# Kernel tuning notes

Hardware: AMD Instinct MI355X
Metric: run time of the kernel (lower is better)

Reference implementation:

```python
import jax, jax.numpy as jnp
import numpy as np

N_HEADS = 8
D_K = 64
NEG = 1e9


def setup_inputs() -> dict:
    key = jax.random.key(0)
    k1, k2, k3 = jax.random.split(key, 3)
    B, L, C = 4, 2048, 512
    x = jax.random.normal(k1, (B, L, C), dtype=jnp.float32)
    W_in = jax.random.normal(k2, (C, N_HEADS * D_K * 3), dtype=jnp.float32) * (C ** -0.5)
    b_in = jnp.zeros((N_HEADS * D_K * 3,), dtype=jnp.float32)
    W_out = jax.random.normal(k3, (N_HEADS * D_K, C), dtype=jnp.float32) * ((N_HEADS * D_K) ** -0.5)
    b_out = jnp.zeros((C,), dtype=jnp.float32)
    return {"x": x, "W_in": W_in, "b_in": b_in, "W_out": W_out, "b_out": b_out}


def reference(x, W_in, b_in, W_out, b_out):
    B, L, C = x.shape
    H, Dk = N_HEADS, D_K
    scale = Dk ** -0.5
    qkv = x @ W_in + b_in                       # [B, L, 3*H*Dk]
    qkv = qkv.reshape(B, L, H, 3 * Dk)
    q, k, v = jnp.split(qkv, 3, axis=-1)         # each [B, L, H, Dk]
    attn = jnp.einsum('bihd,bjhd->bijh', q, k) * scale  # [B, L, L, H]
    mask = jnp.tril(jnp.ones((L, L), dtype=x.dtype))[None, :, :, None]
    attn = attn * mask - NEG * (1.0 - mask)
    attn = jax.nn.softmax(attn, axis=2)          # softmax over j
    res = jnp.einsum('bijh,bjhd->bihd', attn, v)  # [B, L, H, Dk]
    res = res.reshape(B, L, H * Dk)
    res = res @ W_out + b_out
    return res + x
```

## Files before the change

### kernel.cpp

```cpp
#include <hip/hip_runtime.h>
#include <hip/hip_bf16.h>
#include <math.h>
#include <cstddef>
#include <cstring>


constexpr int B_SZ  = 4;
constexpr int L_SEQ = 2048;
constexpr int C_DIM = 512;
constexpr int H_N   = 8;
constexpr int DK    = 64;
constexpr int N_QKV = 1536;
constexpr int M_ROWS = B_SZ * L_SEQ;
constexpr float SCALE = 0.125f;
constexpr float DEFER_THR = 8.f;

typedef __attribute__((ext_vector_type(4))) float f32x4;
typedef __attribute__((ext_vector_type(8))) short bf16x8;
typedef __attribute__((ext_vector_type(4))) unsigned int u32x4;

static __device__ inline ushort f2bf(float f) {
  unsigned u = __builtin_bit_cast(unsigned, f);
  u += 0x7fffu + ((u >> 16) & 1u);
  return (ushort)(u >> 16);
}

static __device__ inline unsigned pack_bf2(float a, float b) {
  const __hip_bfloat162 v = __float22bfloat162_rn(make_float2(a, b));
  unsigned u;
  __builtin_memcpy(&u, &v, 4);
  return u;
}

typedef __attribute__((address_space(1))) const unsigned int* gas1_t;
typedef __attribute__((address_space(3))) unsigned int* las3_t;
static __device__ inline void gload_lds16(const void* g, void* l) {
  __builtin_amdgcn_global_load_lds((gas1_t)g, (las3_t)l, 16, 0, 0);
}


__global__ __launch_bounds__(256) void prep_w(
    const float* __restrict__ W_in, const float* __restrict__ W_out,
    ushort* __restrict__ WinT, ushort* __restrict__ WoutT) {
  __shared__ ushort T[64][65];
  const int id = blockIdx.x;
  const float* src;
  ushort* dst;
  int R, C, c0, r0;
  if (id < 192) {
    src = W_in; dst = WinT; R = C_DIM; C = N_QKV;
    c0 = (id % 24) * 64; r0 = (id / 24) * 64;
  } else {
    const int t = id - 192;
    src = W_out; dst = WoutT; R = C_DIM; C = C_DIM;
    c0 = (t % 8) * 64; r0 = (t / 8) * 64;
  }
#pragma unroll
  for (int p = 0; p < 16; ++p) {
    const int idx = threadIdx.x + p * 256;
    const int r = idx >> 6, c = idx & 63;
    T[r][c] = f2bf(src[(size_t)(r0 + r) * C + c0 + c]);
  }
  __syncthreads();
#pragma unroll
  for (int p = 0; p < 16; ++p) {
    const int idx = threadIdx.x + p * 256;
    const int r = idx >> 6, c = idx & 63;
    dst[(size_t)(c0 + r) * R + r0 + c] = T[c][r];
  }
}

__global__ __launch_bounds__(256) void gemm_qkv(
    const float* __restrict__ Af, const ushort* __restrict__ Bt,
    const float* __restrict__ bias, ushort* __restrict__ Qo,
    ushort* __restrict__ Ko, ushort* __restrict__ Vto, int N, int K, int nbx) {
  __shared__ float Alf[128 * 32];
  __shared__ ushort Bl[128 * 32];
  const int id = blockIdx.x;
  const int xcd = id & 7, i = id >> 3;
  const int bn = (i % nbx) * 128;
  const int bm = (xcd * 8 + i / nbx) * 128;
  const int tid = threadIdx.x;
  const int w = tid >> 6, l = tid & 63;
  const int cc = l & 15, gg = l >> 4;
  const int wr = w >> 1, wc = w & 1;
  f32x4 acc[4][4] = {};

  for (int k0 = 0; k0 < K; k0 += 32) {
#pragma unroll
    for (int q = 0; q < 4; ++q) {
      const int cidx = q * 256 + tid;
      const int row = cidx >> 3, pc = cidx & 7;
      gload_lds16(Af + (size_t)(bm + row) * K + k0 + ((pc ^ (row & 7)) << 2),
                  &Alf[(q * 256 + w * 64) * 4]);
    }
#pragma unroll
    for (int q = 0; q < 2; ++q) {
      const int cbase = q * 256 + w * 64;
      const int c = cbase + l;
      gload_lds16(Bt + (size_t)(bn + (c >> 2)) * K + k0 + (c & 3) * 8,
                  &Bl[cbase * 8]);
    }
    __syncthreads();
    bf16x8 aF[4], bF[4];
#pragma unroll
    for (int i2 = 0; i2 < 4; ++i2) {
      const int rowA = wr * 64 + i2 * 16 + cc;
      const float4 fa = *reinterpret_cast<const float4*>(
          &Alf[rowA * 32 + (((2 * gg) ^ (cc & 7)) << 2)]);
      const float4 fb = *reinterpret_cast<const float4*>(
          &Alf[rowA * 32 + (((2 * gg + 1) ^ (cc & 7)) << 2)]);
      u32x4 up;
      up[0] = pack_bf2(fa.x, fa.y);
      up[1] = pack_bf2(fa.z, fa.w);
      up[2] = pack_bf2(fb.x, fb.y);
      up[3] = pack_bf2(fb.z, fb.w);
      aF[i2] = __builtin_bit_cast(bf16x8, up);
    }
#pragma unroll
    for (int j = 0; j < 4; ++j)
      bF[j] = *reinterpret_cast<const bf16x8*>(
          &Bl[(wc * 64 + j * 16 + cc) * 32 + gg * 8]);
#pragma unroll
    for (int i2 = 0; i2 < 4; ++i2)
#pragma unroll
      for (int j = 0; j < 4; ++j)
        acc[i2][j] = __builtin_amdgcn_mfma_f32_16x16x32_bf16(aF[i2], bF[j],
                                                             acc[i2][j], 0, 0, 0);
    __syncthreads();
  }

#pragma unroll
  for (int j = 0; j < 4; ++j) {
    const int colbase = bn + wc * 64 + j * 16;
    const int h = colbase / 192, rem = colbase % 192;
    const int type = rem / 64, d = (rem % 64) + cc;
    const float bv = bias[colbase + cc];
#pragma unroll
    for (int i2 = 0; i2 < 4; ++i2) {
      const int rowbase = bm + wr * 64 + i2 * 16 + 4 * gg;
      const int b = rowbase >> 11, ll = rowbase & 2047;
      const size_t bh32 = (size_t)(b * H_N + h) * 32;
      if (type == 0) {
#pragma unroll
        for (int r = 0; r < 4; ++r)
          Qo[((size_t)(b * H_N + h) * L_SEQ + ll + r) * DK + d] =
              f2bf(acc[i2][j][r] + bv);
      } else if (type == 1) {
#pragma unroll
        for (int r = 0; r < 4; ++r) {
          const int jg = ll + r;
          Ko[(bh32 + (jg >> 6)) * 4096 + (jg & 63) * 64 +
             (((d >> 3) ^ (jg & 7)) << 3) + (d & 7)] =
              f2bf(acc[i2][j][r] + bv);
        }
      } else {
        ushort4 pk;
        pk.x = f2bf(acc[i2][j][0] + bv);
        pk.y = f2bf(acc[i2][j][1] + bv);
        pk.z = f2bf(acc[i2][j][2] + bv);
        pk.w = f2bf(acc[i2][j][3] + bv);
        const size_t idx = (bh32 + (ll >> 6)) * 4096 + (size_t)d * 64 +
                           ((((ll & 63) >> 3) ^ (d & 7)) << 3) + (ll & 7);
        *reinterpret_cast<ushort4*>(&Vto[idx]) = pk;
      }
    }
  }
}

__global__ __launch_bounds__(256) void gemm_out(
    const ushort* __restrict__ A, const ushort* __restrict__ Bt,
    const float* __restrict__ bias, float* __restrict__ outF,
    const float* __restrict__ resid, int N, int K, int nbx) {
  __shared__ ushort Al[64 * 32];
  __shared__ ushort Bl[64 * 32];
  const int id = blockIdx.x;
  const int xcd = id & 7, i = id >> 3;
  const int bn = (i % nbx) * 64;
  const int bm = (xcd * 16 + i / nbx) * 64;
  const int tid = threadIdx.x;
  const int w = tid >> 6, l = tid & 63;
  const int cc = l & 15, gg = l >> 4;
  const int wr = w >> 1, wc = w & 1;
  f32x4 acc[2][2] = {};

  for (int k0 = 0; k0 < K; k0 += 32) {
    {
      const int c = w * 64 + l;
      gload_lds16(A + (size_t)(bm + (c >> 2)) * K + k0 + (c & 3) * 8,
                  &Al[(w * 64) * 8]);
    }
    {
      const int c = w * 64 + l;
      gload_lds16(Bt + (size_t)(bn + (c >> 2)) * K + k0 + (c & 3) * 8,
                  &Bl[(w * 64) * 8]);
    }
    __syncthreads();
    bf16x8 aF[2], bF[2];
#pragma unroll
    for (int i2 = 0; i2 < 2; ++i2)
      aF[i2] = *reinterpret_cast<const bf16x8*>(
          &Al[(wr * 32 + i2 * 16 + cc) * 32 + gg * 8]);
#pragma unroll
    for (int j = 0; j < 2; ++j)
      bF[j] = *reinterpret_cast<const bf16x8*>(
          &Bl[(wc * 32 + j * 16 + cc) * 32 + gg * 8]);
#pragma unroll
    for (int i2 = 0; i2 < 2; ++i2)
#pragma unroll
      for (int j = 0; j < 2; ++j)
        acc[i2][j] = __builtin_amdgcn_mfma_f32_16x16x32_bf16(aF[i2], bF[j],
                                                             acc[i2][j], 0, 0, 0);
    __syncthreads();
  }

#pragma unroll
  for (int j = 0; j < 2; ++j) {
    const int col = bn + wc * 32 + j * 16 + cc;
    const float bv = bias[col];
#pragma unroll
    for (int i2 = 0; i2 < 2; ++i2) {
      const int rowbase = bm + wr * 32 + i2 * 16 + 4 * gg;
#pragma unroll
      for (int r = 0; r < 4; ++r) {
        const size_t off = (size_t)(rowbase + r) * N + col;
        outF[off] = acc[i2][j][r] + bv + resid[off];
      }
    }
  }
}

#define STAGE(buf, tile)                                                     \
  {                                                                          \
    const ushort* kg_ = KoB + (size_t)(tile) * 4096 + w * 1024 + lane * 8;   \
    const ushort* vg_ = VtB + (size_t)(tile) * 4096 + w * 1024 + lane * 8;   \
    gload_lds16(kg_, &Ks[buf][w * 1024]);                                    \
    gload_lds16(kg_ + 512, &Ks[buf][w * 1024 + 512]);                        \
    gload_lds16(vg_, &Vs[buf][w * 1024]);                                    \
    gload_lds16(vg_ + 512, &Vs[buf][w * 1024 + 512]);                        \
  }

__global__ __launch_bounds__(256, 4) void attn_mfma(
    const ushort* __restrict__ Q, const ushort* __restrict__ Ko,
    const ushort* __restrict__ Vt, ushort* __restrict__ attn_out) {
  __shared__ ushort Ks[2][4096];
  __shared__ ushort Vs[2][4096];
  __shared__ ushort Pw_s[4][1024];
  const int id = blockIdx.x;
  const int bh = (id & 7) + 8 * ((id >> 3) & 3);
  const int qt = 31 - (id >> 5);
  const int tid = threadIdx.x;
  const int w = tid >> 6, lane = tid & 63;
  const int c = lane & 15, g = lane >> 4;
  const int b = bh >> 3, h = bh & 7;
  const ushort* KoB = Ko + (size_t)bh * 32 * 4096;
  const ushort* VtB = Vt + (size_t)bh * 32 * 4096;
  const int q0 = qt * 64 + w * 16;
  ushort* Pw = Pw_s[w];
  const int pc0 = (g ^ (c & 7)) * 8;
  const int pc1 = ((g + 4) ^ (c & 7)) * 8;

  bf16x8 qA[2];
  {
    const ushort* qp = Q + ((size_t)bh * L_SEQ + q0 + c) * DK + g * 8;
    qA[0] = *reinterpret_cast<const bf16x8*>(qp);
    qA[1] = *reinterpret_cast<const bf16x8*>(qp + 32);
  }

  f32x4 O[4] = {};
  float mrow[4] = {-INFINITY, -INFINITY, -INFINITY, -INFINITY};
  float lsum[4] = {};
  const f32x4 zero4 = {0.f, 0.f, 0.f, 0.f};

  STAGE(0, 0);
  __syncthreads();

  for (int jt = 0; jt <= qt; ++jt) {
    const int cur = jt & 1;
    if (jt < qt) STAGE(cur ^ 1, jt + 1);
    const ushort* Kc = Ks[cur];
    const ushort* Vc = Vs[cur];
    const int j0 = jt * 64;
    f32x4 S[4];
#pragma unroll
    for (int n = 0; n < 4; ++n) {
      const bf16x8 k0 = *reinterpret_cast<const bf16x8*>(&Kc[(n * 16 + c) * 64 + pc0]);
      const bf16x8 k1 = *reinterpret_cast<const bf16x8*>(&Kc[(n * 16 + c) * 64 + pc1]);
      S[n] = __builtin_amdgcn_mfma_f32_16x16x32_bf16(qA[0], k0, zero4, 0, 0, 0);
      S[n] = __builtin_amdgcn_mfma_f32_16x16x32_bf16(qA[1], k1, S[n], 0, 0, 0);
    }
    const bool diag = (jt == qt);
#pragma unroll
    for (int n = 0; n < 4; ++n)
#pragma unroll
      for (int r = 0; r < 4; ++r) {
        float v = S[n][r] * SCALE;
        if (diag && (j0 + n * 16 + c) > (q0 + 4 * g + r)) v = -INFINITY;
        S[n][r] = v;
      }
    float pm[4];
    int exceed = 0;
#pragma unroll
    for (int r = 0; r < 4; ++r) {
      pm[r] = fmaxf(fmaxf(S[0][r], S[1][r]), fmaxf(S[2][r], S[3][r]));
      exceed |= (pm[r] > mrow[r] + DEFER_THR);
    }
    if (__any(exceed)) {
#pragma unroll
      for (int r = 0; r < 4; ++r) {
        float fm = pm[r];
        fm = fmaxf(fm, __shfl_xor(fm, 1, 16));
        fm = fmaxf(fm, __shfl_xor(fm, 2, 16));
        fm = fmaxf(fm, __shfl_xor(fm, 4, 16));
        fm = fmaxf(fm, __shfl_xor(fm, 8, 16));
        const float mnew = fmaxf(mrow[r], fm);
        const float corr = __expf(mrow[r] - mnew);
        lsum[r] *= corr;
#pragma unroll
        for (int t = 0; t < 4; ++t) O[t][r] *= corr;
        mrow[r] = mnew;
      }
    }
#pragma unroll
    for (int n = 0; n < 4; ++n)
#pragma unroll
      for (int r = 0; r < 4; ++r) {
        const float p = __expf(S[n][r] - mrow[r]);
        S[n][r] = p;
        lsum[r] += p;
      }
#pragma unroll
    for (int n = 0; n < 4; ++n)
#pragma unroll
      for (int r = 0; r < 4; ++r) {
        const int row = 4 * g + r;
        Pw[row * 64 + ((2 * n + (c >> 3)) ^ (row & 7)) * 8 + (c & 7)] =
            f2bf(S[n][r]);
      }
    const bf16x8 pA0 = *reinterpret_cast<const bf16x8*>(&Pw[c * 64 + pc0]);
    const bf16x8 pA1 = *reinterpret_cast<const bf16x8*>(&Pw[c * 64 + pc1]);
#pragma unroll
    for (int t = 0; t < 4; ++t) {
      const bf16x8 v0 = *reinterpret_cast<const bf16x8*>(&Vc[(t * 16 + c) * 64 + pc0]);
      const bf16x8 v1 = *reinterpret_cast<const bf16x8*>(&Vc[(t * 16 + c) * 64 + pc1]);
      O[t] = __builtin_amdgcn_mfma_f32_16x16x32_bf16(pA0, v0, O[t], 0, 0, 0);
      O[t] = __builtin_amdgcn_mfma_f32_16x16x32_bf16(pA1, v1, O[t], 0, 0, 0);
    }
    __syncthreads();
  }
  float inv[4];
#pragma unroll
  for (int r = 0; r < 4; ++r) {
    float s = lsum[r];
    s += __shfl_xor(s, 1, 16);
    s += __shfl_xor(s, 2, 16);
    s += __shfl_xor(s, 4, 16);
    s += __shfl_xor(s, 8, 16);
    inv[r] = 1.f / s;
  }
#pragma unroll
  for (int t = 0; t < 4; ++t)
#pragma unroll
    for (int r = 0; r < 4; ++r)
      attn_out[((size_t)b * L_SEQ + q0 + 4 * g + r) * C_DIM + h * DK + t * 16 + c] =
          f2bf(O[t][r] * inv[r]);
}

extern "C" void kernel_launch(void* const* d_in, const int* in_sizes, int n_in,
                              void* d_out, int out_size, void* d_ws,
                              size_t ws_size, hipStream_t stream) {
  const float* x     = (const float*)d_in[0];
  const float* W_in  = (const float*)d_in[1];
  const float* b_in  = (const float*)d_in[2];
  const float* W_out = (const float*)d_in[3];
  const float* b_out = (const float*)d_in[4];
  float* out = (float*)d_out;

  ushort* WinT  = (ushort*)d_ws;
  ushort* WoutT = WinT + (size_t)N_QKV * C_DIM;
  ushort* Qo    = WoutT + (size_t)C_DIM * C_DIM;
  ushort* Ko    = Qo + (size_t)M_ROWS * C_DIM;
  ushort* Vto   = Ko + (size_t)M_ROWS * C_DIM;
  ushort* attnb = Vto + (size_t)M_ROWS * C_DIM;

  prep_w<<<dim3(256, 1, 1), 256, 0, stream>>>(W_in, W_out, WinT, WoutT);
  gemm_qkv<<<dim3(768, 1, 1), 256, 0, stream>>>(
      x, WinT, b_in, Qo, Ko, Vto, N_QKV, C_DIM, 12);
  attn_mfma<<<dim3(1024, 1, 1), 256, 0, stream>>>(Qo, Ko, Vto, attnb);
  gemm_out<<<dim3(1024, 1, 1), 256, 0, stream>>>(
      attnb, WoutT, b_out, out, x, C_DIM, C_DIM, 8);
}
```

Baseline: 86.83 us.

## Double-buffer LDS tiles in QKV and output GEMMs to overlap loads

Both projection GEMMs now keep two shared-memory buffers and issue the async global-to-LDS loads for the next K tile before computing on the current one. This is meant to hide global load latency behind the MFMA work. It doubles LDS use per block, which may lower occupancy. Correctness depends on the remaining end-of-iteration barrier and on the compiler inserting the right vmcnt waits for the direct-to-LDS loads.

```diff
diff --git a/kernel.cpp b/kernel.cpp
--- a/kernel.cpp
+++ b/kernel.cpp
@@ -70,12 +70,31 @@
   }
 }
 
+#define STAGE_G1(buf, k0)                                                    \
+  {                                                                          \
+    _Pragma("unroll")                                                        \
+    for (int q_ = 0; q_ < 4; ++q_) {                                         \
+      const int cidx_ = q_ * 256 + tid;                                      \
+      const int row_ = cidx_ >> 3, pc_ = cidx_ & 7;                          \
+      gload_lds16(                                                           \
+          Af + (size_t)(bm + row_) * K + (k0) + ((pc_ ^ (row_ & 7)) << 2),   \
+          &Alf[buf][(q_ * 256 + w * 64) * 4]);                               \
+    }                                                                        \
+    _Pragma("unroll")                                                        \
+    for (int q_ = 0; q_ < 2; ++q_) {                                         \
+      const int cbase_ = q_ * 256 + w * 64;                                  \
+      const int c_ = cbase_ + l;                                             \
+      gload_lds16(Bt + (size_t)(bn + (c_ >> 2)) * K + (k0) + (c_ & 3) * 8,   \
+                  &Bl[buf][cbase_ * 8]);                                     \
+    }                                                                        \
+  }
+
 __global__ __launch_bounds__(256) void gemm_qkv(
     const float* __restrict__ Af, const ushort* __restrict__ Bt,
     const float* __restrict__ bias, ushort* __restrict__ Qo,
     ushort* __restrict__ Ko, ushort* __restrict__ Vto, int N, int K, int nbx) {
-  __shared__ float Alf[128 * 32];
-  __shared__ ushort Bl[128 * 32];
+  __shared__ float Alf[2][128 * 32];
+  __shared__ ushort Bl[2][128 * 32];
   const int id = blockIdx.x;
   const int xcd = id & 7, i = id >> 3;
   const int bn = (i % nbx) * 128;
@@ -85,31 +104,22 @@
   const int cc = l & 15, gg = l >> 4;
   const int wr = w >> 1, wc = w & 1;
   f32x4 acc[4][4] = {};
-
-  for (int k0 = 0; k0 < K; k0 += 32) {
-#pragma unroll
-    for (int q = 0; q < 4; ++q) {
-      const int cidx = q * 256 + tid;
-      const int row = cidx >> 3, pc = cidx & 7;
-      gload_lds16(Af + (size_t)(bm + row) * K + k0 + ((pc ^ (row & 7)) << 2),
-                  &Alf[(q * 256 + w * 64) * 4]);
-    }
-#pragma unroll
-    for (int q = 0; q < 2; ++q) {
-      const int cbase = q * 256 + w * 64;
-      const int c = cbase + l;
-      gload_lds16(Bt + (size_t)(bn + (c >> 2)) * K + k0 + (c & 3) * 8,
-                  &Bl[cbase * 8]);
-    }
-    __syncthreads();
+  const int nk = K / 32;
+
+  STAGE_G1(0, 0);
+  __syncthreads();
+
+  for (int ki = 0; ki < nk; ++ki) {
+    const int cur = ki & 1;
+    if (ki + 1 < nk) STAGE_G1(cur ^ 1, (ki + 1) * 32);
     bf16x8 aF[4], bF[4];
 #pragma unroll
     for (int i2 = 0; i2 < 4; ++i2) {
       const int rowA = wr * 64 + i2 * 16 + cc;
       const float4 fa = *reinterpret_cast<const float4*>(
-          &Alf[rowA * 32 + (((2 * gg) ^ (cc & 7)) << 2)]);
+          &Alf[cur][rowA * 32 + (((2 * gg) ^ (cc & 7)) << 2)]);
       const float4 fb = *reinterpret_cast<const float4*>(
-          &Alf[rowA * 32 + (((2 * gg + 1) ^ (cc & 7)) << 2)]);
+          &Alf[cur][rowA * 32 + (((2 * gg + 1) ^ (cc & 7)) << 2)]);
       u32x4 up;
       up[0] = pack_bf2(fa.x, fa.y);
       up[1] = pack_bf2(fa.z, fa.w);
@@ -120,7 +130,7 @@
 #pragma unroll
     for (int j = 0; j < 4; ++j)
       bF[j] = *reinterpret_cast<const bf16x8*>(
-          &Bl[(wc * 64 + j * 16 + cc) * 32 + gg * 8]);
+          &Bl[cur][(wc * 64 + j * 16 + cc) * 32 + gg * 8]);
 #pragma unroll
     for (int i2 = 0; i2 < 4; ++i2)
 #pragma unroll
@@ -168,12 +178,21 @@
   }
 }
 
+#define STAGE_G2(buf, k0)                                                    \
+  {                                                                          \
+    const int c_ = w * 64 + l;                                               \
+    gload_lds16(A + (size_t)(bm + (c_ >> 2)) * K + (k0) + (c_ & 3) * 8,      \
+                &Al[buf][(w * 64) * 8]);                                     \
+    gload_lds16(Bt + (size_t)(bn + (c_ >> 2)) * K + (k0) + (c_ & 3) * 8,     \
+                &Bl[buf][(w * 64) * 8]);                                     \
+  }
+
 __global__ __launch_bounds__(256) void gemm_out(
     const ushort* __restrict__ A, const ushort* __restrict__ Bt,
     const float* __restrict__ bias, float* __restrict__ outF,
     const float* __restrict__ resid, int N, int K, int nbx) {
-  __shared__ ushort Al[64 * 32];
-  __shared__ ushort Bl[64 * 32];
+  __shared__ ushort Al[2][64 * 32];
+  __shared__ ushort Bl[2][64 * 32];
   const int id = blockIdx.x;
   const int xcd = id & 7, i = id >> 3;
   const int bn = (i % nbx) * 64;
@@ -183,28 +202,23 @@
   const int cc = l & 15, gg = l >> 4;
   const int wr = w >> 1, wc = w & 1;
   f32x4 acc[2][2] = {};
-
-  for (int k0 = 0; k0 < K; k0 += 32) {
-    {
-      const int c = w * 64 + l;
-      gload_lds16(A + (size_t)(bm + (c >> 2)) * K + k0 + (c & 3) * 8,
-                  &Al[(w * 64) * 8]);
-    }
-    {
-      const int c = w * 64 + l;
-      gload_lds16(Bt + (size_t)(bn + (c >> 2)) * K + k0 + (c & 3) * 8,
-                  &Bl[(w * 64) * 8]);
-    }
-    __syncthreads();
+  const int nk = K / 32;
+
+  STAGE_G2(0, 0);
+  __syncthreads();
+
+  for (int ki = 0; ki < nk; ++ki) {
+    const int cur = ki & 1;
+    if (ki + 1 < nk) STAGE_G2(cur ^ 1, (ki + 1) * 32);
     bf16x8 aF[2], bF[2];
 #pragma unroll
     for (int i2 = 0; i2 < 2; ++i2)
       aF[i2] = *reinterpret_cast<const bf16x8*>(
-          &Al[(wr * 32 + i2 * 16 + cc) * 32 + gg * 8]);
+          &Al[cur][(wr * 32 + i2 * 16 + cc) * 32 + gg * 8]);
 #pragma unroll
     for (int j = 0; j < 2; ++j)
       bF[j] = *reinterpret_cast<const bf16x8*>(
-          &Bl[(wc * 32 + j * 16 + cc) * 32 + gg * 8]);
+          &Bl[cur][(wc * 32 + j * 16 + cc) * 32 + gg * 8]);
 #pragma unroll
     for (int i2 = 0; i2 < 2; ++i2)
 #pragma unroll
```

New measurement: 88.21 us. No clear change (+1.6%).
